# Kernel optimization log

Measured on AMD Instinct MI355X. Metric: run time of the kernel, lower is better.

The kernel has to match this reference:

```python
import jax, jax.numpy as jnp
import numpy as np

N, E, IN, H0, H1 = 50000, 1600000, 64, 64, 128


def _gcn(h, W, b, row, col):
    # PyG GCNConv, add_self_loops=False, unit edge weights:
    # out[col] += d^{-1/2}[row] * d^{-1/2}[col] * (h @ W)[row]; bias added after aggregation
    n = h.shape[0]
    deg = jnp.zeros((n,), h.dtype).at[col].add(jnp.ones((row.shape[0],), h.dtype))
    dinv = jnp.where(deg > 0, jax.lax.rsqrt(jnp.maximum(deg, 1e-12)), 0.0)
    norm = (dinv[row] * dinv[col])[:, None]  # [E,1]
    m = h @ W  # transform before propagate (small GEMM)
    out = jnp.zeros((n, W.shape[1]), h.dtype).at[col].add(norm * m[row])
    return out + b


def _bn(h, g, b):
    # BatchNorm1d training-mode math (biased variance), eps=1e-5
    mu = h.mean(0)
    var = ((h - mu) ** 2).mean(0)
    return g * (h - mu) * jax.lax.rsqrt(var + 1e-5) + b


def _san(h):
    return jnp.nan_to_num(h, nan=0.0, posinf=100.0, neginf=-100.0)


def _slice(x, ei, W0, b0, W1, b1, res1, g0, be0, g1, be1):
    row, col = ei[0], ei[1]
    # layer 0: conv -> bn -> relu -> (dropout=eval identity) -> residual (Identity, 64==64) -> nan_to_num
    h1 = _san(jax.nn.relu(_bn(_gcn(x, W0, b0, row, col), g0, be0)) + x)
    # layer 1 (last): conv -> bn -> residual (Linear proj 64->128, no bias) -> nan_to_num
    h2 = _san(_bn(_gcn(h1, W1, b1, row, col), g1, be1) + h1 @ res1)
    return h2


def setup_inputs() -> dict:
    k = jax.random.split(jax.random.key(0), 16)
    f = lambda kk, sh, s: jax.random.normal(kk, sh, jnp.float32) * s
    return {
        "x": f(k[0], (N, IN), 1.0),
        "edge_index0": jax.random.randint(k[1], (2, E), 0, N),
        "edge_index1": jax.random.randint(k[2], (2, E), 0, N),
        "w0_s0": f(k[3], (IN, H0), 0.1), "b0_s0": jnp.zeros((H0,), jnp.float32),
        "w1_s0": f(k[4], (H0, H1), 0.1), "b1_s0": jnp.zeros((H1,), jnp.float32),
        "res1_s0": f(k[5], (H0, H1), 0.1),
        "w0_s1": f(k[6], (IN, H0), 0.1), "b0_s1": jnp.zeros((H0,), jnp.float32),
        "w1_s1": f(k[7], (H0, H1), 0.1), "b1_s1": jnp.zeros((H1,), jnp.float32),
        "res1_s1": f(k[8], (H0, H1), 0.1),
        "bn_g0": jnp.ones((H0,), jnp.float32), "bn_b0": jnp.zeros((H0,), jnp.float32),
        "bn_g1": jnp.ones((H1,), jnp.float32), "bn_b1": jnp.zeros((H1,), jnp.float32),
        "fc1_w": f(k[9], (2 * H1, H1), 0.1), "fc1_b": jnp.zeros((H1,), jnp.float32),
        "fc2_w": f(k[10], (H1, 2), 0.1), "fc2_b": jnp.zeros((2,), jnp.float32),
    }


def reference(x, edge_index0, edge_index1,
              w0_s0, b0_s0, w1_s0, b1_s0, res1_s0,
              w0_s1, b0_s1, w1_s1, b1_s1, res1_s1,
              bn_g0, bn_b0, bn_g1, bn_b1,
              fc1_w, fc1_b, fc2_w, fc2_b):
    out0 = _slice(x, edge_index0, w0_s0, b0_s0, w1_s0, b1_s0, res1_s0, bn_g0, bn_b0, bn_g1, bn_b1)
    out1 = _slice(x, edge_index1, w0_s1, b0_s1, w1_s1, b1_s1, res1_s1, bn_g0, bn_b0, bn_g1, bn_b1)
    combined = jnp.concatenate([out0, out1], axis=1)  # [N, 2*H1]
    h = jax.nn.relu(combined @ fc1_w + fc1_b)  # dropout is eval-mode identity
    logits = h @ fc2_w + fc2_b
    return logits, jax.nn.softmax(logits, axis=1)
```

## Files before the change

### kernel.cpp

```cpp
#include <hip/hip_runtime.h>
#include <hip/hip_bf16.h>
#include <math.h>


typedef short v8s __attribute__((ext_vector_type(8)));
typedef float f32x4 __attribute__((ext_vector_type(4)));

#define BSTRIDE 10240

__device__ __forceinline__ float sanf(float v) {
    if (v != v) return 0.f;
    if (isinf(v)) return v > 0.f ? 100.f : -100.f;
    return v;
}

__device__ __forceinline__ unsigned short bf16of(float v) {
    __hip_bfloat16 h = __float2bfloat16(v);
    return *(unsigned short*)&h;
}
__device__ __forceinline__ unsigned pack2(float lo, float hi) {
    return (unsigned)bf16of(lo) | ((unsigned)bf16of(hi) << 16);
}
__device__ __forceinline__ float uflo(unsigned u) { return __uint_as_float(u << 16); }
__device__ __forceinline__ float ufhi(unsigned u) { return __uint_as_float(u & 0xFFFF0000u); }
__device__ __forceinline__ float fofbf16(unsigned short u) {
    return __uint_as_float(((unsigned)u) << 16);
}

__device__ __forceinline__ void packone(const float* __restrict__ src, unsigned* __restrict__ dst,
                                        int L, int Khalf, int F) {
    int c = L / Khalf, kp = L - c * Khalf;
    dst[L] = pack2(src[(2 * kp) * F + c], src[(2 * kp + 1) * F + c]);
}

__global__ __launch_bounds__(256) void prep_kernel(const float* __restrict__ w0_0,
                                                   const float* __restrict__ w0_1,
                                                   const float* __restrict__ w1_0,
                                                   const float* __restrict__ w1_1,
                                                   const float* __restrict__ r_0,
                                                   const float* __restrict__ r_1,
                                                   const float* __restrict__ fc1,
                                                   unsigned* __restrict__ wpk,
                                                   int* __restrict__ bcnt,
                                                   float* __restrict__ sums) {
    int gid = blockIdx.x * 256 + threadIdx.x;
    if (gid < 512) bcnt[gid] = 0;
    if (gid < 8192) sums[gid] = 0.f;
    if (gid < 2048)       packone(w0_0, wpk + 0,     gid - 0,     32, 64);
    else if (gid < 4096)  packone(w0_1, wpk + 2048,  gid - 2048,  32, 64);
    else if (gid < 8192)  packone(w1_0, wpk + 4096,  gid - 4096,  32, 128);
    else if (gid < 12288) packone(w1_1, wpk + 8192,  gid - 8192,  32, 128);
    else if (gid < 16384) packone(r_0,  wpk + 12288, gid - 12288, 32, 128);
    else if (gid < 20480) packone(r_1,  wpk + 16384, gid - 16384, 32, 128);
    else if (gid < 36864) packone(fc1,  wpk + 20480, gid - 20480, 128, 128);
}


__global__ __launch_bounds__(512) void kC_bin(const int* __restrict__ ei0,
                                              const int* __restrict__ ei1,
                                              int* __restrict__ bcnt,
                                              unsigned* __restrict__ binned,
                                              int E, int n) {
    __shared__ int cnt[512];
    __shared__ int base[512];
    int t = threadIdx.x;
    cnt[t] = 0;
    int E2 = 2 * E;
    int e0 = blockIdx.x * 8192;
    unsigned pk[16];
    int bk[16];
    __syncthreads();
#pragma unroll
    for (int j = 0; j < 16; ++j) {
        int ge = e0 + t + j * 512;
        bk[j] = -1;
        if (ge < E2) {
            int slice = ge >= E;
            const int* ei = slice ? ei1 : ei0;
            int e = ge - slice * E;
            int col = ei[E + e], row = ei[e];
            int gcol = slice * n + col;
            bk[j] = gcol >> 8;
            pk[j] = (unsigned)row | (((unsigned)gcol & 255u) << 16);
            atomicAdd(&cnt[bk[j]], 1);
        }
    }
    __syncthreads();
    {
        int c = cnt[t];
        base[t] = c ? atomicAdd(&bcnt[t], c) : 0;
    }
    __syncthreads();
    cnt[t] = 0;
    __syncthreads();
#pragma unroll
    for (int j = 0; j < 16; ++j) {
        if (bk[j] >= 0) {
            int loc = atomicAdd(&cnt[bk[j]], 1);
            int off = base[bk[j]] + loc;
            if (off < BSTRIDE) binned[(size_t)bk[j] * BSTRIDE + off] = pk[j];
        }
    }
}

__global__ __launch_bounds__(256) void kB_scan(const int* __restrict__ bcnt,
                                               int* __restrict__ bstart, int NB) {
    __shared__ int tmp[256];
    int t = threadIdx.x, carry = 0;
    for (int bse = 0; bse < NB; bse += 256) {
        int i = bse + t;
        int v = (i < NB) ? bcnt[i] : 0;
        tmp[t] = v;
        __syncthreads();
        for (int off = 1; off < 256; off <<= 1) {
            int u = (t >= off) ? tmp[t - off] : 0;
            __syncthreads();
            tmp[t] += u;
            __syncthreads();
        }
        if (i < NB) bstart[i] = tmp[t] - v + carry;
        carry += tmp[255];
        __syncthreads();
    }
    if (t == 0) bstart[NB] = carry;
}

__global__ __launch_bounds__(512) void kD_build(const unsigned* __restrict__ binned,
                                                const int* __restrict__ bstart,
                                                int* __restrict__ rowptr,
                                                float* __restrict__ dinv,
                                                unsigned short* __restrict__ csr,
                                                int n2, int NB) {
    __shared__ int cnt[256];
    __shared__ int scn[256];
    __shared__ int cur[256];
    int b = blockIdx.x, t = threadIdx.x;
    int s = bstart[b], e = bstart[b + 1];
    int m = e - s;
    const unsigned* seg = binned + (size_t)b * BSTRIDE;
    if (t < 256) cnt[t] = 0;
    __syncthreads();
    for (int i = t; i < m; i += 512) atomicAdd(&cnt[(seg[i] >> 16) & 255], 1);
    __syncthreads();
    int v = (t < 256) ? cnt[t] : 0;
    if (t < 256) scn[t] = v;
    __syncthreads();
    for (int off = 1; off < 256; off <<= 1) {
        int u = (t < 256 && t >= off) ? scn[t - off] : 0;
        __syncthreads();
        if (t < 256) scn[t] += u;
        __syncthreads();
    }
    if (t < 256) {
        int excl = scn[t] - v;
        int gcol = b * 256 + t;
        if (gcol < n2) {
            rowptr[gcol] = s + excl;
            dinv[gcol] = v > 0 ? rsqrtf((float)v) : 0.f;
        }
        cur[t] = excl;
    }
    __syncthreads();
    for (int i = t; i < m; i += 512) {
        unsigned p = seg[i];
        int cl = (p >> 16) & 255;
        int pos = s + atomicAdd(&cur[cl], 1);
        csr[pos] = (unsigned short)(p & 0xFFFFu);
    }
    if (b == 0 && t == 0) rowptr[n2] = bstart[NB];
}


__global__ __launch_bounds__(256) void prescale_bf(const float* __restrict__ x,
                                                   const float* __restrict__ dinv,
                                                   unsigned short* __restrict__ xsb,
                                                   int n64, int n) {
    int i8 = (blockIdx.x * 256 + threadIdx.x) * 8;
    if (i8 >= n64) return;
    int row = i8 >> 6;
    float4 v0 = *(const float4*)&x[i8];
    float4 v1 = *(const float4*)&x[i8 + 4];
    float d0 = dinv[row], d1 = dinv[n + row];
    uint4 o0, o1;
    o0.x = pack2(v0.x * d0, v0.y * d0); o0.y = pack2(v0.z * d0, v0.w * d0);
    o0.z = pack2(v1.x * d0, v1.y * d0); o0.w = pack2(v1.z * d0, v1.w * d0);
    o1.x = pack2(v0.x * d1, v0.y * d1); o1.y = pack2(v0.z * d1, v0.w * d1);
    o1.z = pack2(v1.x * d1, v1.y * d1); o1.w = pack2(v1.z * d1, v1.w * d1);
    *(uint4*)&xsb[i8] = o0;
    *(uint4*)&xsb[n64 + i8] = o1;
}

__global__ __launch_bounds__(256) void gatherbf_kernel(const int* __restrict__ rowptr,
                                                       const unsigned short* __restrict__ csr,
                                                       const unsigned short* __restrict__ m,
                                                       const float* __restrict__ dinv,
                                                       unsigned short* __restrict__ outb,
                                                       int n, int n2) {
    int gid = blockIdx.x * 256 + threadIdx.x;
    int node = gid >> 3;
    if (node >= n2) return;
    int l = threadIdx.x & 7;
    const unsigned short* mb = m + (size_t)((node >= n) ? n : 0) * 64;
    int s = rowptr[node], e = rowptr[node + 1];
    float a0 = 0.f, a1 = 0.f, a2 = 0.f, a3 = 0.f, a4 = 0.f, a5 = 0.f, a6 = 0.f, a7 = 0.f;
    int b = s;
    for (; b + 8 <= e; b += 8) {
        int idx = csr[b + l];
        uint4 u[8];
#pragma unroll
        for (int j = 0; j < 8; ++j) {
            int r = __shfl(idx, j, 8);
            u[j] = *(const uint4*)&mb[(size_t)r * 64 + l * 8];
        }
#pragma unroll
        for (int j = 0; j < 8; ++j) {
            a0 += uflo(u[j].x); a1 += ufhi(u[j].x);
            a2 += uflo(u[j].y); a3 += ufhi(u[j].y);
            a4 += uflo(u[j].z); a5 += ufhi(u[j].z);
            a6 += uflo(u[j].w); a7 += ufhi(u[j].w);
        }
    }
    if (b < e) {
        int cntn = e - b;
        int idx = (b + l < e) ? (int)csr[b + l] : 0;
        for (int j = 0; j < cntn; ++j) {
            int r = __shfl(idx, j, 8);
            uint4 u = *(const uint4*)&mb[(size_t)r * 64 + l * 8];
            a0 += uflo(u.x); a1 += ufhi(u.x);
            a2 += uflo(u.y); a3 += ufhi(u.y);
            a4 += uflo(u.z); a5 += ufhi(u.z);
            a6 += uflo(u.w); a7 += ufhi(u.w);
        }
    }
    float d = dinv[node];
    uint4 o;
    o.x = pack2(a0 * d, a1 * d);
    o.y = pack2(a2 * d, a3 * d);
    o.z = pack2(a4 * d, a5 * d);
    o.w = pack2(a6 * d, a7 * d);
    *(uint4*)&outb[(size_t)node * 64 + l * 8] = o;
}


template <int F>
__global__ __launch_bounds__(256) void mfma_gemmb(const unsigned short* __restrict__ Ab,
                                                  const unsigned* __restrict__ WT0,
                                                  const unsigned* __restrict__ WT1,
                                                  unsigned short* __restrict__ Cb,
                                                  float* __restrict__ sums_base,
                                                  int roff, int n) {
    constexpr int NC = F / 16;
    __shared__ float ls[2 * F];
    __shared__ unsigned short stb[64 * F];
    int BPS = (n + 63) >> 6;
    int slice = blockIdx.x >= BPS;
    int sb = blockIdx.x - slice * BPS;
    const unsigned* WT = slice ? WT1 : WT0;
    int row0 = slice * n + sb * 64;
    int rows = min(64, n - sb * 64);
    for (int i = threadIdx.x; i < 2 * F; i += 256) ls[i] = 0.f;
    int w = threadIdx.x >> 6, lane = threadIdx.x & 63, q = lane >> 4, ln = lane & 15;
    const unsigned* A32 = (const unsigned*)Ab;
    size_t arow = (size_t)(row0 + 16 * w + ln) * 32;
    v8s af0 = *(const v8s*)&A32[arow + q * 4];
    v8s af1 = *(const v8s*)&A32[arow + 16 + q * 4];
    f32x4 acc[NC];
#pragma unroll
    for (int ct = 0; ct < NC; ++ct) acc[ct] = {0.f, 0.f, 0.f, 0.f};
#pragma unroll
    for (int ct = 0; ct < NC; ++ct) {
        v8s b0 = *(const v8s*)&WT[(ct * 16 + ln) * 32 + q * 4];
        v8s b1 = *(const v8s*)&WT[(ct * 16 + ln) * 32 + 16 + q * 4];
        acc[ct] = __builtin_amdgcn_mfma_f32_16x16x32_bf16(af0, b0, acc[ct], 0, 0, 0);
        acc[ct] = __builtin_amdgcn_mfma_f32_16x16x32_bf16(af1, b1, acc[ct], 0, 0, 0);
    }
    __syncthreads();
#pragma unroll
    for (int ct = 0; ct < NC; ++ct) {
        float s1 = 0.f, s2 = 0.f;
        int cc = ct * 16 + ln;
#pragma unroll
        for (int i = 0; i < 4; ++i) {
            int r = 16 * w + q * 4 + i;
            stb[r * F + (cc ^ ((r & 7) << 3))] = bf16of(acc[ct][i]);
            if (r < rows) {
                float v = acc[ct][i];
                s1 += v;
                s2 += v * v;
            }
        }
        s1 += __shfl_xor(s1, 16); s1 += __shfl_xor(s1, 32);
        s2 += __shfl_xor(s2, 16); s2 += __shfl_xor(s2, 32);
        if (q == 0) {
            atomicAdd(&ls[cc], s1);
            atomicAdd(&ls[F + cc], s2);
        }
    }
    __syncthreads();
    {
        constexpr int CPT = F / 4;
        int rr = threadIdx.x >> 2, sg = threadIdx.x & 3;
        if (rr < rows) {
            int swz = (rr & 7) << 3;
            int cb = sg * CPT;
            uint4* dst = (uint4*)(Cb + (size_t)(row0 + rr) * F + cb);
#pragma unroll
            for (int jj = 0; jj < CPT / 8; ++jj)
                dst[jj] = *(const uint4*)&stb[rr * F + ((cb + jj * 8) ^ swz)];
        }
    }
    if (threadIdx.x < F) {
        float* dst = sums_base + (blockIdx.x & 7) * 1024 + roff + slice * 2 * F;
        unsafeAtomicAdd(&dst[threadIdx.x], ls[threadIdx.x]);
        unsafeAtomicAdd(&dst[F + threadIdx.x], ls[F + threadIdx.x]);
    }
}

__global__ __launch_bounds__(256) void mfma_apply1(const unsigned short* __restrict__ h1b,
                                                   const unsigned short* __restrict__ Tb,
                                                   const unsigned* __restrict__ RT0,
                                                   const unsigned* __restrict__ RT1,
                                                   const float* __restrict__ scsh,
                                                   unsigned short* __restrict__ comb, int n) {
    __shared__ float st[64 * 128];
    int BPS = (n + 63) >> 6;
    int slice = blockIdx.x >= BPS;
    int sb = blockIdx.x - slice * BPS;
    const unsigned* WT = slice ? RT1 : RT0;
    int row0 = slice * n + sb * 64;
    int rows = min(64, n - sb * 64);
    int w = threadIdx.x >> 6, lane = threadIdx.x & 63, q = lane >> 4, ln = lane & 15;
    const unsigned* A32 = (const unsigned*)h1b;
    size_t arow = (size_t)(row0 + 16 * w + ln) * 32;
    v8s af0 = *(const v8s*)&A32[arow + q * 4];
    v8s af1 = *(const v8s*)&A32[arow + 16 + q * 4];
    f32x4 acc[8];
#pragma unroll
    for (int ct = 0; ct < 8; ++ct) acc[ct] = {0.f, 0.f, 0.f, 0.f};
#pragma unroll
    for (int ct = 0; ct < 8; ++ct) {
        v8s b0 = *(const v8s*)&WT[(ct * 16 + ln) * 32 + q * 4];
        v8s b1 = *(const v8s*)&WT[(ct * 16 + ln) * 32 + 16 + q * 4];
        acc[ct] = __builtin_amdgcn_mfma_f32_16x16x32_bf16(af0, b0, acc[ct], 0, 0, 0);
        acc[ct] = __builtin_amdgcn_mfma_f32_16x16x32_bf16(af1, b1, acc[ct], 0, 0, 0);
    }
#pragma unroll
    for (int ct = 0; ct < 8; ++ct) {
        int cc = ct * 16 + ln;
#pragma unroll
        for (int i = 0; i < 4; ++i) {
            int r = 16 * w + q * 4 + i;
            st[r * 128 + (cc ^ ((r & 7) << 2))] = acc[ct][i];
        }
    }
    __syncthreads();
    int rr = threadIdx.x >> 2, sg = threadIdx.x & 3;
    if (rr >= rows) return;
    int swz = (rr & 7) << 2;
    int rg = row0 + rr;
    const uint4* tbp = (const uint4*)(Tb + (size_t)rg * 128 + sg * 32);
    const float* scb = scsh + slice * 256 + sg * 32;
    uint4* outp = (uint4*)(comb + (size_t)(rg - slice * n) * 256 + slice * 128 + sg * 32);
#pragma unroll
    for (int jj = 0; jj < 4; ++jj) {
        uint4 t = tbp[jj];
        int base = sg * 32 + jj * 8;
        float4 a0 = *(const float4*)&st[rr * 128 + (base ^ swz)];
        float4 a1 = *(const float4*)&st[rr * 128 + ((base + 4) ^ swz)];
        float4 s0 = *(const float4*)&scb[jj * 8];
        float4 s1 = *(const float4*)&scb[jj * 8 + 4];
        float4 h0 = *(const float4*)&scb[128 + jj * 8];
        float4 h1v = *(const float4*)&scb[128 + jj * 8 + 4];
        float o0 = sanf(fmaf(uflo(t.x), s0.x, h0.x) + a0.x);
        float o1 = sanf(fmaf(ufhi(t.x), s0.y, h0.y) + a0.y);
        float o2 = sanf(fmaf(uflo(t.y), s0.z, h0.z) + a0.z);
        float o3 = sanf(fmaf(ufhi(t.y), s0.w, h0.w) + a0.w);
        float o4 = sanf(fmaf(uflo(t.z), s1.x, h1v.x) + a1.x);
        float o5 = sanf(fmaf(ufhi(t.z), s1.y, h1v.y) + a1.y);
        float o6 = sanf(fmaf(uflo(t.w), s1.z, h1v.z) + a1.z);
        float o7 = sanf(fmaf(ufhi(t.w), s1.w, h1v.w) + a1.w);
        uint4 ov;
        ov.x = pack2(o0, o1);
        ov.y = pack2(o2, o3);
        ov.z = pack2(o4, o5);
        ov.w = pack2(o6, o7);
        outp[jj] = ov;
    }
}

__global__ __launch_bounds__(256) void mfma_head_fc2(const unsigned short* __restrict__ comb,
                                                     const unsigned* __restrict__ FT,
                                                     const float* __restrict__ bias,
                                                     const float* __restrict__ w2,
                                                     const float* __restrict__ b2,
                                                     float* __restrict__ out, int n) {
    int row0 = blockIdx.x * 64;
    int rows = min(64, n - row0);
    int w = threadIdx.x >> 6, lane = threadIdx.x & 63, q = lane >> 4, ln = lane & 15;
    const unsigned* A32 = (const unsigned*)comb;
    size_t arow = (size_t)(row0 + 16 * w + ln) * 128;
    f32x4 acc[8];
#pragma unroll
    for (int ct = 0; ct < 8; ++ct) acc[ct] = {0.f, 0.f, 0.f, 0.f};
#pragma unroll
    for (int kt = 0; kt < 4; ++kt) {
        v8s af0 = *(const v8s*)&A32[arow + kt * 32 + q * 4];
        v8s af1 = *(const v8s*)&A32[arow + kt * 32 + 16 + q * 4];
#pragma unroll
        for (int ct = 0; ct < 8; ++ct) {
            v8s b0 = *(const v8s*)&FT[(ct * 16 + ln) * 128 + kt * 32 + q * 4];
            v8s b1 = *(const v8s*)&FT[(ct * 16 + ln) * 128 + kt * 32 + 16 + q * 4];
            acc[ct] = __builtin_amdgcn_mfma_f32_16x16x32_bf16(af0, b0, acc[ct], 0, 0, 0);
            acc[ct] = __builtin_amdgcn_mfma_f32_16x16x32_bf16(af1, b1, acc[ct], 0, 0, 0);
        }
    }
    float p0[4] = {0.f, 0.f, 0.f, 0.f}, p1[4] = {0.f, 0.f, 0.f, 0.f};
#pragma unroll
    for (int ct = 0; ct < 8; ++ct) {
        int c = ct * 16 + ln;
        float bi = bias[c];
        float w20 = w2[c * 2], w21 = w2[c * 2 + 1];
#pragma unroll
        for (int i = 0; i < 4; ++i) {
            float h = fmaxf(acc[ct][i] + bi, 0.f);
            p0[i] = fmaf(h, w20, p0[i]);
            p1[i] = fmaf(h, w21, p1[i]);
        }
    }
#pragma unroll
    for (int i = 0; i < 4; ++i) {
#pragma unroll
        for (int msk = 1; msk < 16; msk <<= 1) {
            p0[i] += __shfl_xor(p0[i], msk);
            p1[i] += __shfl_xor(p1[i], msk);
        }
    }
    if (ln == 0) {
        float bb0 = b2[0], bb1 = b2[1];
#pragma unroll
        for (int i = 0; i < 4; ++i) {
            int r = 16 * w + q * 4 + i;
            if (r >= rows) continue;
            int R = row0 + r;
            float l0 = p0[i] + bb0, l1 = p1[i] + bb1;
            float mx = fmaxf(l0, l1);
            float e0 = expf(l0 - mx), e1 = expf(l1 - mx);
            float inv = 1.0f / (e0 + e1);
            out[(size_t)R * 2] = l0;
            out[(size_t)R * 2 + 1] = l1;
            out[(size_t)2 * n + R * 2] = e0 * inv;
            out[(size_t)2 * n + R * 2 + 1] = e1 * inv;
        }
    }
}


template <int F>
__global__ void bnfinal_kernel(const float* __restrict__ sums_base, int roff,
                               const float* __restrict__ g,
                               const float* __restrict__ be, float* __restrict__ scsh, int n) {
    int f = threadIdx.x;
    if (f >= F) return;
    int slice = blockIdx.x;
    float s1 = 0.f, s2 = 0.f;
#pragma unroll
    for (int r = 0; r < 8; ++r) {
        const float* src = sums_base + r * 1024 + roff + slice * 2 * F;
        s1 += src[f];
        s2 += src[F + f];
    }
    float inv_n = 1.0f / (float)n;
    float mu = s1 * inv_n;
    float var = fmaxf(s2 * inv_n - mu * mu, 0.f);
    float scale = g[f] * rsqrtf(var + 1e-5f);
    scsh[slice * 2 * F + f] = scale;
    scsh[slice * 2 * F + F + f] = be[f] - mu * scale;
}

__global__ __launch_bounds__(256) void apply0_kernel(const unsigned short* __restrict__ t0b,
                                                     const float* __restrict__ x,
                                                     const float* __restrict__ scsh,
                                                     const float* __restrict__ dinv,
                                                     unsigned short* __restrict__ h1b,
                                                     unsigned short* __restrict__ h1sb,
                                                     int n64, int total) {
    int i8 = (blockIdx.x * 256 + threadIdx.x) * 8;
    if (i8 >= total) return;
    int slice = i8 >= n64;
    int f0 = i8 & 63;
    const float* sc = scsh + slice * 128;
    uint4 t = *(const uint4*)&t0b[i8];
    const float* xp = x + (i8 - slice * n64);
    float4 x0 = *(const float4*)xp;
    float4 x1 = *(const float4*)(xp + 4);
    float4 s0 = *(const float4*)&sc[f0];
    float4 s1 = *(const float4*)&sc[f0 + 4];
    float4 g0 = *(const float4*)&sc[64 + f0];
    float4 g1 = *(const float4*)&sc[64 + f0 + 4];
    float d = dinv[i8 >> 6];
    float tv[8] = {uflo(t.x), ufhi(t.x), uflo(t.y), ufhi(t.y),
                   uflo(t.z), ufhi(t.z), uflo(t.w), ufhi(t.w)};
    float sa[8] = {s0.x, s0.y, s0.z, s0.w, s1.x, s1.y, s1.z, s1.w};
    float sh[8] = {g0.x, g0.y, g0.z, g0.w, g1.x, g1.y, g1.z, g1.w};
    float xv[8] = {x0.x, x0.y, x0.z, x0.w, x1.x, x1.y, x1.z, x1.w};
    unsigned po[4], ps[4];
#pragma unroll
    for (int j = 0; j < 4; ++j) {
        float a = sanf(fmaxf(fmaf(tv[2 * j], sa[2 * j], sh[2 * j]), 0.f) + xv[2 * j]);
        float b = sanf(fmaxf(fmaf(tv[2 * j + 1], sa[2 * j + 1], sh[2 * j + 1]), 0.f) + xv[2 * j + 1]);
        po[j] = pack2(a, b);
        ps[j] = pack2(a * d, b * d);
    }
    *(uint4*)&h1b[i8] = *(uint4*)po;
    *(uint4*)&h1sb[i8] = *(uint4*)ps;
}

static inline int cdiv(int a, int b) { return (a + b - 1) / b; }

extern "C" void kernel_launch(void* const* d_in, const int* in_sizes, int n_in,
                              void* d_out, int out_size, void* d_ws, size_t ws_size,
                              hipStream_t stream) {
    const float* x       = (const float*)d_in[0];
    const int*   ei0     = (const int*)d_in[1];
    const int*   ei1     = (const int*)d_in[2];
    const float* w0_s0   = (const float*)d_in[3];
    const float* w1_s0   = (const float*)d_in[5];
    const float* res1_s0 = (const float*)d_in[7];
    const float* w0_s1   = (const float*)d_in[8];
    const float* w1_s1   = (const float*)d_in[10];
    const float* res1_s1 = (const float*)d_in[12];
    const float* bn_g0   = (const float*)d_in[13];
    const float* bn_b0   = (const float*)d_in[14];
    const float* bn_g1   = (const float*)d_in[15];
    const float* bn_b1   = (const float*)d_in[16];
    const float* fc1_w   = (const float*)d_in[17];
    const float* fc1_b   = (const float*)d_in[18];
    const float* fc2_w   = (const float*)d_in[19];
    const float* fc2_b   = (const float*)d_in[20];
    float* out = (float*)d_out;

    int n = in_sizes[0] / 64;
    int E = in_sizes[1] / 2;
    int n2 = 2 * n, E2 = 2 * E;
    int n64 = n * 64;
    int NB = cdiv(n2, 256);
    int BPS = cdiv(n, 64);

    float* X1 = (float*)d_ws;
    float* S  = X1 + (size_t)n2 * 64;
    unsigned short* Gb   = (unsigned short*)(S + (size_t)n2 * 64);
    unsigned short* h1b  = Gb + (size_t)n2 * 64;
    unsigned short* comb = h1b + (size_t)n2 * 64;
    unsigned short* xsb  = comb + (size_t)n * 256;
    float* dinv = (float*)(xsb + (size_t)n * 128);
    float* sums = dinv + n2;
    float* scsh = sums + 8192;
    unsigned* wpk = (unsigned*)(scsh + 512);
    unsigned short* csr = (unsigned short*)(wpk + 36864);
    int* rowptr = (int*)(csr + (size_t)E2);
    int* bcnt   = rowptr + (n2 + 1);
    int* bstart = bcnt + 512;
    unsigned short* t0b = (unsigned short*)X1;
    unsigned short* Tb  = (unsigned short*)X1;
    unsigned* binned = (unsigned*)comb;
    unsigned short* h1sb = (unsigned short*)S;
    unsigned* w0T0 = wpk + 0,    *w0T1 = wpk + 2048;
    unsigned* w1T0 = wpk + 4096, *w1T1 = wpk + 8192;
    unsigned* rT0  = wpk + 12288,*rT1  = wpk + 16384;
    unsigned* fT   = wpk + 20480;

    prep_kernel<<<144, 256, 0, stream>>>(w0_s0, w0_s1, w1_s0, w1_s1,
                                         res1_s0, res1_s1, fc1_w, wpk, bcnt, sums);
    kC_bin<<<cdiv(E2, 8192), 512, 0, stream>>>(ei0, ei1, bcnt, binned, E, n);
    kB_scan<<<1, 256, 0, stream>>>(bcnt, bstart, NB);
    kD_build<<<NB, 512, 0, stream>>>(binned, bstart, rowptr, dinv, csr, n2, NB);

    prescale_bf<<<cdiv(n64, 2048), 256, 0, stream>>>(x, dinv, xsb, n64, n);
    gatherbf_kernel<<<cdiv(n2 * 8, 256), 256, 0, stream>>>(rowptr, csr, xsb, dinv, Gb, n, n2);
    mfma_gemmb<64><<<2 * BPS, 256, 0, stream>>>(Gb, w0T0, w0T1, t0b, sums, 512, n);
    bnfinal_kernel<64><<<2, 64, 0, stream>>>(sums, 512, bn_g0, bn_b0, scsh, n);
    apply0_kernel<<<cdiv(2 * n64, 2048), 256, 0, stream>>>(t0b, x, scsh, dinv, h1b, h1sb, n64, 2 * n64);

    gatherbf_kernel<<<cdiv(n2 * 8, 256), 256, 0, stream>>>(rowptr, csr, h1sb, dinv, Gb, n, n2);
    mfma_gemmb<128><<<2 * BPS, 256, 0, stream>>>(Gb, w1T0, w1T1, Tb, sums, 0, n);
    bnfinal_kernel<128><<<2, 128, 0, stream>>>(sums, 0, bn_g1, bn_b1, scsh, n);
    mfma_apply1<<<2 * BPS, 256, 0, stream>>>(h1b, Tb, rT0, rT1, scsh, comb, n);

    mfma_head_fc2<<<BPS, 256, 0, stream>>>(comb, fT, fc1_b, fc2_w, fc2_b, out, n);
}
```

Before: 372.5 us.

## Double-buffer gather loads and map slices to XCD groups in gather kernel

The gather kernel now software-pipelines neighbor row loads with two 8-deep register buffers, so the next batch of loads is in flight while the current batch is accumulated. Tail batches are zero-padded instead of handled by a scalar remainder loop. Block indices are remapped so the blocks on XCDs 0-3 process slice 0 and those on XCDs 4-7 process slice 1, which is meant to keep each slice's source features in fewer L2 caches. The cost is roughly double the register use for loads, which may lower occupancy.

```diff
diff --git a/kernel.cpp b/kernel.cpp
--- a/kernel.cpp
+++ b/kernel.cpp
@@ -190,47 +190,79 @@
     *(uint4*)&xsb[n64 + i8] = o1;
 }
 
+#define LOAD8(U, IDX)                                                       \
+    do {                                                                    \
+        _Pragma("unroll") for (int j = 0; j < 8; ++j) {                     \
+            int r = __shfl((IDX), j, 8);                                    \
+            (U)[j] = *(const uint4*)&mb[(size_t)r * 64 + l * 8];            \
+        }                                                                   \
+    } while (0)
+#define ZPAD8(U, BB)                                                        \
+    do {                                                                    \
+        _Pragma("unroll") for (int j = 0; j < 8; ++j)                       \
+            if ((BB) + j >= e) { (U)[j].x = 0; (U)[j].y = 0;                \
+                                 (U)[j].z = 0; (U)[j].w = 0; }              \
+    } while (0)
+#define ACC8(U)                                                             \
+    do {                                                                    \
+        _Pragma("unroll") for (int j = 0; j < 8; ++j) {                     \
+            a0 += uflo((U)[j].x); a1 += ufhi((U)[j].x);                     \
+            a2 += uflo((U)[j].y); a3 += ufhi((U)[j].y);                     \
+            a4 += uflo((U)[j].z); a5 += ufhi((U)[j].z);                     \
+            a6 += uflo((U)[j].w); a7 += ufhi((U)[j].w);                     \
+        }                                                                   \
+    } while (0)
+
 __global__ __launch_bounds__(256) void gatherbf_kernel(const int* __restrict__ rowptr,
                                                        const unsigned short* __restrict__ csr,
-                                                       const unsigned short* __restrict__ m,
+                                                       const unsigned short* __restrict__ xsb,
                                                        const float* __restrict__ dinv,
                                                        unsigned short* __restrict__ outb,
-                                                       int n, int n2) {
-    int gid = blockIdx.x * 256 + threadIdx.x;
-    int node = gid >> 3;
-    if (node >= n2) return;
+                                                       int n) {
+    int blk = blockIdx.x;
+    int xcd = blk & 7;
+    int slice = (xcd >= 4) ? 1 : 0;
+    int rank = (blk >> 3) * 4 + (xcd & 3);
+    int nodeLocal = rank * 32 + (threadIdx.x >> 3);
+    if (nodeLocal >= n) return;
+    int node = slice * n + nodeLocal;
     int l = threadIdx.x & 7;
-    const unsigned short* mb = m + (size_t)((node >= n) ? n : 0) * 64;
+    const unsigned short* mb = xsb + (size_t)slice * n * 64;
     int s = rowptr[node], e = rowptr[node + 1];
     float a0 = 0.f, a1 = 0.f, a2 = 0.f, a3 = 0.f, a4 = 0.f, a5 = 0.f, a6 = 0.f, a7 = 0.f;
+    uint4 uA[8], uB[8];
     int b = s;
-    for (; b + 8 <= e; b += 8) {
-        int idx = csr[b + l];
-        uint4 u[8];
-#pragma unroll
-        for (int j = 0; j < 8; ++j) {
-            int r = __shfl(idx, j, 8);
-            u[j] = *(const uint4*)&mb[(size_t)r * 64 + l * 8];
-        }
-#pragma unroll
-        for (int j = 0; j < 8; ++j) {
-            a0 += uflo(u[j].x); a1 += ufhi(u[j].x);
-            a2 += uflo(u[j].y); a3 += ufhi(u[j].y);
-            a4 += uflo(u[j].z); a5 += ufhi(u[j].z);
-            a6 += uflo(u[j].w); a7 += ufhi(u[j].w);
-        }
-    }
-    if (b < e) {
-        int cntn = e - b;
-        int idx = (b + l < e) ? (int)csr[b + l] : 0;
-        for (int j = 0; j < cntn; ++j) {
-            int r = __shfl(idx, j, 8);
-            uint4 u = *(const uint4*)&mb[(size_t)r * 64 + l * 8];
-            a0 += uflo(u.x); a1 += ufhi(u.x);
-            a2 += uflo(u.y); a3 += ufhi(u.y);
-            a4 += uflo(u.z); a5 += ufhi(u.z);
-            a6 += uflo(u.w); a7 += ufhi(u.w);
-        }
+    if (b + 8 <= e) {
+        int ia = csr[b + l];
+        LOAD8(uA, ia);
+        int bB = b + 8;
+        int ib = (bB + l < e) ? (int)csr[bB + l] : 0;
+        while (true) {
+            bool hasB = (bB < e);
+            if (hasB) {
+                LOAD8(uB, ib);
+                if (bB + 8 > e) ZPAD8(uB, bB);
+            }
+            int bA2 = bB + 8;
+            if (bA2 < e) ia = (bA2 + l < e) ? (int)csr[bA2 + l] : 0;
+            ACC8(uA);
+            if (!hasB) break;
+            bool hasA2 = (bA2 < e);
+            if (hasA2) {
+                LOAD8(uA, ia);
+                if (bA2 + 8 > e) ZPAD8(uA, bA2);
+            }
+            int bB2 = bA2 + 8;
+            if (bB2 < e) ib = (bB2 + l < e) ? (int)csr[bB2 + l] : 0;
+            ACC8(uB);
+            if (!hasA2) break;
+            bB = bB2;
+        }
+    } else if (b < e) {
+        int ia = (b + l < e) ? (int)csr[b + l] : 0;
+        LOAD8(uA, ia);
+        ZPAD8(uA, b);
+        ACC8(uA);
     }
     float d = dinv[node];
     uint4 o;
@@ -545,6 +577,7 @@
     int n64 = n * 64;
     int NB = cdiv(n2, 256);
     int BPS = cdiv(n, 64);
+    int GB = 8 * cdiv(cdiv(n, 32), 4);
 
     float* X1 = (float*)d_ws;
     float* S  = X1 + (size_t)n2 * 64;
@@ -576,12 +609,12 @@
     kD_build<<<NB, 512, 0, stream>>>(binned, bstart, rowptr, dinv, csr, n2, NB);
 
     prescale_bf<<<cdiv(n64, 2048), 256, 0, stream>>>(x, dinv, xsb, n64, n);
-    gatherbf_kernel<<<cdiv(n2 * 8, 256), 256, 0, stream>>>(rowptr, csr, xsb, dinv, Gb, n, n2);
+    gatherbf_kernel<<<GB, 256, 0, stream>>>(rowptr, csr, xsb, dinv, Gb, n);
     mfma_gemmb<64><<<2 * BPS, 256, 0, stream>>>(Gb, w0T0, w0T1, t0b, sums, 512, n);
     bnfinal_kernel<64><<<2, 64, 0, stream>>>(sums, 512, bn_g0, bn_b0, scsh, n);
     apply0_kernel<<<cdiv(2 * n64, 2048), 256, 0, stream>>>(t0b, x, scsh, dinv, h1b, h1sb, n64, 2 * n64);
 
-    gatherbf_kernel<<<cdiv(n2 * 8, 256), 256, 0, stream>>>(rowptr, csr, h1sb, dinv, Gb, n, n2);
+    gatherbf_kernel<<<GB, 256, 0, stream>>>(rowptr, csr, h1sb, dinv, Gb, n);
     mfma_gemmb<128><<<2 * BPS, 256, 0, stream>>>(Gb, w1T0, w1T1, Tb, sums, 0, n);
     bnfinal_kernel<128><<<2, 128, 0, stream>>>(sums, 0, bn_g1, bn_b1, scsh, n);
     mfma_apply1<<<2 * BPS, 256, 0, stream>>>(h1b, Tb, rT0, rT1, scsh, comb, n);
```

After: 363.8 us. 2.3% less time.
